# Optimization experiments

Measured on AMD Instinct MI355X. Metric: run time of the kernel, lower is better.

## Reference

```python
import jax, jax.numpy as jnp
import numpy as np

ALPHA = 0.2  # LeakyReLU negative slope


def setup_inputs() -> dict:
    key = jax.random.key(0)
    k1, k2, k3, k4 = jax.random.split(key, 4)
    N, IN, H, D = 4096, 256, 8, 32
    h = jax.random.normal(k1, (N, IN), dtype=jnp.float32)
    adj = jax.random.randint(k2, (N, N), 0, 2, dtype=jnp.int32)
    W = jax.random.normal(k3, (H, IN, D), dtype=jnp.float32) * 0.074  # ~xavier gain 1.414
    a = jax.random.normal(k4, (H, 2 * D, 1), dtype=jnp.float32) * 0.23
    return {"h": h, "adj": adj, "W": W, "a": a}


def reference(h, adj, W, a):
    # h: [N, IN], adj: [N, N], W: [H, IN, D], a: [H, 2D, 1]
    H, IN, D = W.shape
    Wh = jnp.einsum('ni,hid->hnd', h, W)              # [H, N, D]
    a1 = a[:, :D, 0]                                   # [H, D]
    a2 = a[:, D:, 0]                                   # [H, D]
    Wh1 = jnp.einsum('hnd,hd->hn', Wh, a1)             # [H, N]
    Wh2 = jnp.einsum('hnd,hd->hn', Wh, a2)             # [H, N]
    e = Wh1[:, :, None] + Wh2[:, None, :]              # [H, N, N]
    e = jax.nn.leaky_relu(e, negative_slope=ALPHA)
    mask = (adj > 0)[None, :, :]                       # [1, N, N]
    e = jnp.where(mask, e, -jnp.inf)
    attention = jax.nn.softmax(e, axis=-1)             # [H, N, N]
    # dropout omitted (eval mode / deterministic)
    h_prime = jnp.einsum('hij,hjd->hid', attention, Wh)  # [H, N, D]
    # concat heads: [N, H*D]
    N = h.shape[0]
    return jnp.transpose(h_prime, (1, 0, 2)).reshape(N, H * D)
```

## Files before the change

kernel.cpp:

```cpp
#include <hip/hip_runtime.h>
#include <hip/hip_bf16.h>
#include <stdint.h>

#define GAT_ALPHA 0.2f
#define LOG2E 1.4426950408889634f

typedef __attribute__((ext_vector_type(8))) short bf16x8;
typedef __attribute__((ext_vector_type(8))) unsigned short ushort8;
typedef __attribute__((ext_vector_type(4))) float f32x4;
typedef __attribute__((ext_vector_type(4))) unsigned int u32x4;

#if __has_builtin(__builtin_amdgcn_exp2f)
#define EXP2F(x) __builtin_amdgcn_exp2f(x)
#else
#define EXP2F(x) exp2f(x)
#endif

static __device__ __forceinline__ unsigned int cvt_pk_bf16(float a, float b) {
    unsigned int r;
    asm("v_cvt_pk_bf16_f32 %0, %1, %2" : "=v"(r) : "v"(a), "v"(b));
    return r;
}

static __device__ __forceinline__ void gl16(const void* g, void* l) {
    __builtin_amdgcn_global_load_lds((const __attribute__((address_space(1))) void*)g,
                                     (__attribute__((address_space(3))) void*)l, 16, 0, 0);
}

__global__ __launch_bounds__(256) void k_pack_adj(const int* __restrict__ adj,
                                                  unsigned long long* __restrict__ packed,
                                                  int nwords) {
    int gid = blockIdx.x * 256 + threadIdx.x;
    int wid = gid >> 6;
    int lane = threadIdx.x & 63;
    if (wid >= nwords) return;
    int v = adj[(size_t)wid * 64 + lane];
    unsigned long long m = __ballot(v > 0);
    if (lane == 0) packed[wid] = m;
}

__global__ __launch_bounds__(256) void k_cvtW(const float* __restrict__ W,
                                              unsigned short* __restrict__ wbfT) {
    int idx = (blockIdx.x * 256 + threadIdx.x) * 8;
    int hd = idx >> 8;
    int i0 = idx & 255;
    int hh = hd >> 5, dd = hd & 31;
    float v[8];
    #pragma unroll
    for (int k = 0; k < 8; ++k) v[k] = W[((size_t)hh * 256 + i0 + k) * 32 + dd];
    u32x4 o = { cvt_pk_bf16(v[0], v[1]), cvt_pk_bf16(v[2], v[3]),
                cvt_pk_bf16(v[4], v[5]), cvt_pk_bf16(v[6], v[7]) };
    *(u32x4*)&wbfT[idx] = o;
}

__global__ __launch_bounds__(256) void k_wh2(const float* __restrict__ hmat,
                                             const unsigned short* __restrict__ wbfT,
                                             const float* __restrict__ avec,
                                             float* __restrict__ wh1s,
                                             float* __restrict__ wh2s,
                                             unsigned short* __restrict__ whT) {
    const int head = blockIdx.y;
    const int nbase = blockIdx.x * 64;
    const int t = threadIdx.x, w = t >> 6, lane = t & 63;
    const int r = lane & 15, q = lane >> 4;
    const int node0 = nbase + w * 16;

    f32x4 acc0 = {0.f, 0.f, 0.f, 0.f};
    f32x4 acc1 = {0.f, 0.f, 0.f, 0.f};
    const float* arow = &hmat[(size_t)(node0 + r) * 256];
    const unsigned short* b0p = &wbfT[((size_t)head * 32 + r) * 256];
    const unsigned short* b1p = b0p + 16 * 256;
    #pragma unroll
    for (int kt = 0; kt < 8; ++kt) {
        const int ko = kt * 32 + q * 8;
        float4 h0 = *(const float4*)&arow[ko];
        float4 h1 = *(const float4*)&arow[ko + 4];
        u32x4 ap = { cvt_pk_bf16(h0.x, h0.y), cvt_pk_bf16(h0.z, h0.w),
                     cvt_pk_bf16(h1.x, h1.y), cvt_pk_bf16(h1.z, h1.w) };
        bf16x8 af = __builtin_bit_cast(bf16x8, ap);
        bf16x8 b0 = *(const bf16x8*)&b0p[ko];
        bf16x8 b1 = *(const bf16x8*)&b1p[ko];
        acc0 = __builtin_amdgcn_mfma_f32_16x16x32_bf16(af, b0, acc0, 0, 0, 0);
        acc1 = __builtin_amdgcn_mfma_f32_16x16x32_bf16(af, b1, acc1, 0, 0, 0);
    }
    u32x4 pk = { cvt_pk_bf16(acc0[0], acc0[1]), cvt_pk_bf16(acc0[2], acc0[3]),
                 cvt_pk_bf16(acc1[0], acc1[1]), cvt_pk_bf16(acc1[2], acc1[3]) };
    unsigned long long lo = ((unsigned long long)pk[1] << 32) | pk[0];
    unsigned long long hi = ((unsigned long long)pk[3] << 32) | pk[2];
    *(unsigned long long*)&whT[((size_t)head * 32 + r) * 4096 + node0 + q * 4] = lo;
    *(unsigned long long*)&whT[((size_t)head * 32 + 16 + r) * 4096 + node0 + q * 4] = hi;

    float a1lo = avec[head * 64 + r],      a1hi = avec[head * 64 + 16 + r];
    float a2lo = avec[head * 64 + 32 + r], a2hi = avec[head * 64 + 48 + r];
    f32x4 d1, d2;
    #pragma unroll
    for (int i = 0; i < 4; ++i) {
        d1[i] = fmaf(acc0[i], a1lo, acc1[i] * a1hi);
        d2[i] = fmaf(acc0[i], a2lo, acc1[i] * a2hi);
    }
    #pragma unroll
    for (int s = 1; s < 16; s <<= 1) {
        #pragma unroll
        for (int i = 0; i < 4; ++i) {
            d1[i] += __shfl_xor(d1[i], s);
            d2[i] += __shfl_xor(d2[i], s);
        }
    }
    if (r == 0) {
        f32x4 o1 = d1 * LOG2E, o2 = d2 * LOG2E;
        *(f32x4*)&wh1s[(size_t)head * 4096 + node0 + q * 4] = o1;
        *(f32x4*)&wh2s[(size_t)head * 4096 + node0 + q * 4] = o2;
    }
}

__global__ __launch_bounds__(256, 4) void k_attn(const unsigned long long* __restrict__ adj64,
                                                 const float* __restrict__ wh1s,
                                                 const float* __restrict__ wh2s,
                                                 const unsigned short* __restrict__ whT,
                                                 float* __restrict__ out) {
    const int head = blockIdx.y;
    const int rowbase = blockIdx.x * 32;
    const int t = threadIdx.x;
    const int w = t >> 6;
    const int lane = t & 63;
    const int rt = w & 1;
    const int jh = w >> 1;
    const int r = lane & 15;
    const int q = lane >> 4;
    const int row = rowbase + rt * 16 + r;

    __shared__ unsigned short whTl[2][2][32][128];
    __shared__ float wh2t[2][2][128];
    __shared__ float wmxb[4];

    const int ghh = w >> 1;
    const int grg = (w & 1) * 4;
    const unsigned short* gsrc[4];
    #pragma unroll
    for (int c = 0; c < 4; ++c) {
        int d = (grg + c) * 4 + (lane >> 4);
        int p = lane & 15;
        int ls = (p & 8) | ((p ^ d) & 7);
        gsrc[c] = whT + ((size_t)(head * 32 + d)) * 4096 + ghh * 2048 + ls * 8;
    }
    const float* wh2p = &wh2s[(size_t)head * 4096];
    const float* wh2src = wh2p + (lane >> 5) * 2048 + (lane & 31) * 4;

    #pragma unroll
    for (int c = 0; c < 4; ++c)
        gl16(gsrc[c], &whTl[0][ghh][(grg + c) * 4][0]);
    if (w == 0) gl16(wh2src, &wh2t[0][0][0]);

    float lm = -INFINITY;
    #pragma unroll
    for (int kk = 0; kk < 4; ++kk) {
        float4 v = *(const float4*)&wh2p[kk * 1024 + t * 4];
        lm = fmaxf(fmaxf(lm, fmaxf(v.x, v.y)), fmaxf(v.z, v.w));
    }
    #pragma unroll
    for (int s = 1; s < 64; s <<= 1) lm = fmaxf(lm, __shfl_xor(lm, s));
    if (lane == 0) wmxb[w] = lm;
    __syncthreads();
    const float wm = fmaxf(fmaxf(wmxb[0], wmxb[1]), fmaxf(wmxb[2], wmxb[3]));

    const float wh1 = wh1s[(size_t)head * 4096 + row];
    const float sm0 = wh1 + wm;
    const float m = fmaxf(sm0, GAT_ALPHA * sm0);
    const float wh1m = wh1 - m;
    const float c2 = GAT_ALPHA * wh1 - m;

    f32x4 acc0 = {0.f, 0.f, 0.f, 0.f};
    f32x4 acc1 = {0.f, 0.f, 0.f, 0.f};
    f32x4 accd = {0.f, 0.f, 0.f, 0.f};

    const u32x4 onesu = {0x3F803F80u, 0x3F803F80u, 0x3F803F80u, 0x3F803F80u};
    const bf16x8 ones = __builtin_bit_cast(bf16x8, onesu);

    const unsigned long long* arow = adj64 + (size_t)row * 64 + jh * 32;
    unsigned long long au0 = arow[0], au1 = arow[1];
    int cur = 0;

    for (int step = 0; step < 16; ++step) {
        unsigned long long an0 = 0, an1 = 0;
        if (step < 15) {
            #pragma unroll
            for (int c = 0; c < 4; ++c)
                gl16(gsrc[c] + (step + 1) * 128, &whTl[cur ^ 1][ghh][(grg + c) * 4][0]);
            if (w == 0) gl16(wh2src + (step + 1) * 128, &wh2t[cur ^ 1][0][0]);
            an0 = arow[(step + 1) * 2];
            an1 = arow[(step + 1) * 2 + 1];
        }

        #pragma unroll
        for (int kk = 0; kk < 4; ++kk) {
            const int jl = kk * 32 + q * 8;
            const int slot = ((kk * 4 + q) ^ (r & 7)) * 8;
            bf16x8 b0 = *(const bf16x8*)&whTl[cur][jh][r][slot];
            bf16x8 b1 = *(const bf16x8*)&whTl[cur][jh][16 + r][slot];
            unsigned int bits =
                (unsigned int)(((kk < 2 ? au0 : au1) >> ((kk & 1) * 32 + q * 8)) & 0xffull);
            float w2[8];
            *(float4*)&w2[0] = *(const float4*)&wh2t[cur][jh][jl];
            *(float4*)&w2[4] = *(const float4*)&wh2t[cur][jh][jl + 4];

            float p[8];
            #pragma unroll
            for (int b = 0; b < 8; ++b) {
                float u = wh1m + w2[b];
                float tv = fmaf(GAT_ALPHA, w2[b], c2);
                float s = fmaxf(u, tv);
                float pe = EXP2F(s);
                p[b] = (bits & (1u << b)) ? pe : 0.f;
            }
            u32x4 pk = { cvt_pk_bf16(p[0], p[1]), cvt_pk_bf16(p[2], p[3]),
                         cvt_pk_bf16(p[4], p[5]), cvt_pk_bf16(p[6], p[7]) };
            bf16x8 af = __builtin_bit_cast(bf16x8, pk);
            acc0 = __builtin_amdgcn_mfma_f32_16x16x32_bf16(af, b0, acc0, 0, 0, 0);
            acc1 = __builtin_amdgcn_mfma_f32_16x16x32_bf16(af, b1, acc1, 0, 0, 0);
            accd = __builtin_amdgcn_mfma_f32_16x16x32_bf16(af, ones, accd, 0, 0, 0);
        }

        __syncthreads();
        au0 = an0;
        au1 = an1;
        cur ^= 1;
    }

    f32x4* red = (f32x4*)whTl;
    if (jh == 1) {
        f32x4* rp = red + (rt * 64 + lane) * 3;
        rp[0] = acc0;
        rp[1] = acc1;
        rp[2] = accd;
    }
    __syncthreads();
    if (jh == 0) {
        const f32x4* rp = red + (rt * 64 + lane) * 3;
        acc0 += rp[0];
        acc1 += rp[1];
        accd += rp[2];
        #pragma unroll
        for (int i = 0; i < 4; ++i) {
            float inv = 1.0f / accd[i];
            int orow = rowbase + rt * 16 + 4 * q + i;
            out[(size_t)orow * 256 + head * 32 + r]      = acc0[i] * inv;
            out[(size_t)orow * 256 + head * 32 + 16 + r] = acc1[i] * inv;
        }
    }
}

extern "C" void kernel_launch(void* const* d_in, const int* in_sizes, int n_in,
                              void* d_out, int out_size, void* d_ws, size_t ws_size,
                              hipStream_t stream) {
    const float* h   = (const float*)d_in[0];
    const int*   adj = (const int*)d_in[1];
    const float* W   = (const float*)d_in[2];
    const float* a   = (const float*)d_in[3];
    float* out = (float*)d_out;

    char* ws = (char*)d_ws;
    unsigned long long* packed = (unsigned long long*)ws;
    float* wh1s = (float*)(ws + (2 << 20));
    float* wh2s = (float*)(ws + (2 << 20) + (128 << 10));
    unsigned short* whT  = (unsigned short*)(ws + (2 << 20) + (256 << 10));
    unsigned short* wbfT = (unsigned short*)(ws + (4 << 20) + (256 << 10));

    const int nwords = 4096 * 64;
    k_pack_adj<<<nwords * 64 / 256, 256, 0, stream>>>(adj, packed, nwords);
    k_cvtW<<<32, 256, 0, stream>>>(W, wbfT);
    k_wh2<<<dim3(64, 8), 256, 0, stream>>>(h, wbfT, a, wh1s, wh2s, whT);
    k_attn<<<dim3(128, 8), 256, 0, stream>>>(packed, wh1s, wh2s, whT, out);
}
```

Baseline: 85.54 us.

## Precompute per-head Wh2 max via atomics and use packed f32 math in attention

Moves the per-head maximum of the scaled Wh2 scores out of every attention block. It is now computed once in the projection kernel with an order-preserving integer atomicMax, so each k_attn block no longer reads 4096 floats and runs a block reduction before starting. The inner logit computation also uses v_pk_add_f32/v_pk_fma_f32 to handle two elements per instruction. The cost is an extra memset, a few global atomics, and inline asm that may constrain the compiler's scheduling.

```diff
diff --git a/kernel.cpp b/kernel.cpp
--- a/kernel.cpp
+++ b/kernel.cpp
@@ -8,6 +8,7 @@
 typedef __attribute__((ext_vector_type(8))) short bf16x8;
 typedef __attribute__((ext_vector_type(8))) unsigned short ushort8;
 typedef __attribute__((ext_vector_type(4))) float f32x4;
+typedef __attribute__((ext_vector_type(2))) float f32x2;
 typedef __attribute__((ext_vector_type(4))) unsigned int u32x4;
 
 #if __has_builtin(__builtin_amdgcn_exp2f)
@@ -20,6 +21,17 @@
     unsigned int r;
     asm("v_cvt_pk_bf16_f32 %0, %1, %2" : "=v"(r) : "v"(a), "v"(b));
     return r;
+}
+
+static __device__ __forceinline__ f32x2 pk_add(f32x2 a, f32x2 b) {
+    f32x2 d;
+    asm("v_pk_add_f32 %0, %1, %2" : "=v"(d) : "v"(a), "v"(b));
+    return d;
+}
+static __device__ __forceinline__ f32x2 pk_fma(f32x2 a, f32x2 b, f32x2 c) {
+    f32x2 d;
+    asm("v_pk_fma_f32 %0, %1, %2, %3" : "=v"(d) : "v"(a), "v"(b), "v"(c));
+    return d;
 }
 
 static __device__ __forceinline__ void gl16(const void* g, void* l) {
@@ -58,7 +70,8 @@
                                              const float* __restrict__ avec,
                                              float* __restrict__ wh1s,
                                              float* __restrict__ wh2s,
-                                             unsigned short* __restrict__ whT) {
+                                             unsigned short* __restrict__ whT,
+                                             unsigned int* __restrict__ wmax) {
     const int head = blockIdx.y;
     const int nbase = blockIdx.x * 64;
     const int t = threadIdx.x, w = t >> 6, lane = t & 63;
@@ -110,6 +123,14 @@
         f32x4 o1 = d1 * LOG2E, o2 = d2 * LOG2E;
         *(f32x4*)&wh1s[(size_t)head * 4096 + node0 + q * 4] = o1;
         *(f32x4*)&wh2s[(size_t)head * 4096 + node0 + q * 4] = o2;
+        float lmx = fmaxf(fmaxf(o2[0], o2[1]), fmaxf(o2[2], o2[3]));
+        lmx = fmaxf(lmx, __shfl_xor(lmx, 16));
+        lmx = fmaxf(lmx, __shfl_xor(lmx, 32));
+        if (lane == 0) {
+            int i = __float_as_int(lmx);
+            unsigned int u = (i >= 0) ? ((unsigned int)i | 0x80000000u) : ~(unsigned int)i;
+            atomicMax(&wmax[head], u);
+        }
     }
 }
 
@@ -117,6 +138,7 @@
                                                  const float* __restrict__ wh1s,
                                                  const float* __restrict__ wh2s,
                                                  const unsigned short* __restrict__ whT,
+                                                 const unsigned int* __restrict__ wmax,
                                                  float* __restrict__ out) {
     const int head = blockIdx.y;
     const int rowbase = blockIdx.x * 32;
@@ -131,7 +153,6 @@
 
     __shared__ unsigned short whTl[2][2][32][128];
     __shared__ float wh2t[2][2][128];
-    __shared__ float wmxb[4];
 
     const int ghh = w >> 1;
     const int grg = (w & 1) * 4;
@@ -151,23 +172,18 @@
         gl16(gsrc[c], &whTl[0][ghh][(grg + c) * 4][0]);
     if (w == 0) gl16(wh2src, &wh2t[0][0][0]);
 
-    float lm = -INFINITY;
-    #pragma unroll
-    for (int kk = 0; kk < 4; ++kk) {
-        float4 v = *(const float4*)&wh2p[kk * 1024 + t * 4];
-        lm = fmaxf(fmaxf(lm, fmaxf(v.x, v.y)), fmaxf(v.z, v.w));
-    }
-    #pragma unroll
-    for (int s = 1; s < 64; s <<= 1) lm = fmaxf(lm, __shfl_xor(lm, s));
-    if (lane == 0) wmxb[w] = lm;
-    __syncthreads();
-    const float wm = fmaxf(fmaxf(wmxb[0], wmxb[1]), fmaxf(wmxb[2], wmxb[3]));
+    const unsigned int wmu = wmax[head];
+    const float wm = __int_as_float((wmu & 0x80000000u) ? (int)(wmu & 0x7FFFFFFFu)
+                                                        : ~(int)wmu);
 
     const float wh1 = wh1s[(size_t)head * 4096 + row];
     const float sm0 = wh1 + wm;
     const float m = fmaxf(sm0, GAT_ALPHA * sm0);
     const float wh1m = wh1 - m;
     const float c2 = GAT_ALPHA * wh1 - m;
+    const f32x2 wh1m2 = {wh1m, wh1m};
+    const f32x2 al2   = {GAT_ALPHA, GAT_ALPHA};
+    const f32x2 c22   = {c2, c2};
 
     f32x4 acc0 = {0.f, 0.f, 0.f, 0.f};
     f32x4 acc1 = {0.f, 0.f, 0.f, 0.f};
@@ -179,6 +195,8 @@
     const unsigned long long* arow = adj64 + (size_t)row * 64 + jh * 32;
     unsigned long long au0 = arow[0], au1 = arow[1];
     int cur = 0;
+
+    __syncthreads();
 
     for (int step = 0; step < 16; ++step) {
         unsigned long long an0 = 0, an1 = 0;
@@ -199,18 +217,21 @@
             bf16x8 b1 = *(const bf16x8*)&whTl[cur][jh][16 + r][slot];
             unsigned int bits =
                 (unsigned int)(((kk < 2 ? au0 : au1) >> ((kk & 1) * 32 + q * 8)) & 0xffull);
-            float w2[8];
-            *(float4*)&w2[0] = *(const float4*)&wh2t[cur][jh][jl];
-            *(float4*)&w2[4] = *(const float4*)&wh2t[cur][jh][jl + 4];
+            f32x2 wp[4];
+            *(f32x4*)&wp[0] = *(const f32x4*)&wh2t[cur][jh][jl];
+            *(f32x4*)&wp[2] = *(const f32x4*)&wh2t[cur][jh][jl + 4];
 
             float p[8];
             #pragma unroll
-            for (int b = 0; b < 8; ++b) {
-                float u = wh1m + w2[b];
-                float tv = fmaf(GAT_ALPHA, w2[b], c2);
-                float s = fmaxf(u, tv);
-                float pe = EXP2F(s);
-                p[b] = (bits & (1u << b)) ? pe : 0.f;
+            for (int k2 = 0; k2 < 4; ++k2) {
+                f32x2 u  = pk_add(wp[k2], wh1m2);
+                f32x2 tv = pk_fma(al2, wp[k2], c22);
+                float s0 = fmaxf(u.x, tv.x);
+                float s1 = fmaxf(u.y, tv.y);
+                float e0 = EXP2F(s0);
+                float e1 = EXP2F(s1);
+                p[2 * k2]     = (bits & (1u << (2 * k2)))     ? e0 : 0.f;
+                p[2 * k2 + 1] = (bits & (1u << (2 * k2 + 1))) ? e1 : 0.f;
             }
             u32x4 pk = { cvt_pk_bf16(p[0], p[1]), cvt_pk_bf16(p[2], p[3]),
                          cvt_pk_bf16(p[4], p[5]), cvt_pk_bf16(p[6], p[7]) };
@@ -264,10 +285,12 @@
     float* wh2s = (float*)(ws + (2 << 20) + (128 << 10));
     unsigned short* whT  = (unsigned short*)(ws + (2 << 20) + (256 << 10));
     unsigned short* wbfT = (unsigned short*)(ws + (4 << 20) + (256 << 10));
-
+    unsigned int* wmax   = (unsigned int*)(ws + (4 << 20) + (384 << 10));
+
+    hipMemsetAsync(wmax, 0, 8 * sizeof(unsigned int), stream);
     const int nwords = 4096 * 64;
     k_pack_adj<<<nwords * 64 / 256, 256, 0, stream>>>(adj, packed, nwords);
     k_cvtW<<<32, 256, 0, stream>>>(W, wbfT);
-    k_wh2<<<dim3(64, 8), 256, 0, stream>>>(h, wbfT, a, wh1s, wh2s, whT);
-    k_attn<<<dim3(128, 8), 256, 0, stream>>>(packed, wh1s, wh2s, whT, out);
-}
+    k_wh2<<<dim3(64, 8), 256, 0, stream>>>(h, wbfT, a, wh1s, wh2s, whT, wmax);
+    k_attn<<<dim3(128, 8), 256, 0, stream>>>(packed, wh1s, wh2s, whT, wmax, out);
+}
```

After: 120.1 us. +40.4%, slower.
